# Kernel optimization log

Measured on AMD Instinct MI355X. Metric: run time of the kernel, lower is better.

## Reference

```python
import jax, jax.numpy as jnp
import numpy as np

HS = 2048   # hidden_size
NH = 16     # num_attention_heads
HD = HS // NH  # head_dim = 128
FD = 256    # feature_dim
EPS = 1e-5  # layer_norm_epsilon


def setup_inputs() -> dict:
    key = jax.random.key(0)
    ks = jax.random.split(key, 12)
    s = 0.02
    return {
        "hidden_states": jax.random.normal(ks[0], (2, 4096, HS), jnp.float32),
        "attention_mask": jnp.zeros((2, 4096), jnp.float32),
        "Wq": jax.random.normal(ks[1], (HS, HS), jnp.float32) * s,
        "bq": jnp.zeros((HS,), jnp.float32),
        "Wk": jax.random.normal(ks[2], (HS, HS), jnp.float32) * s,
        "bk": jnp.zeros((HS,), jnp.float32),
        "Wv": jax.random.normal(ks[3], (HS, HS), jnp.float32) * s,
        "bv": jnp.zeros((HS,), jnp.float32),
        "Wo": jax.random.normal(ks[4], (HS, HS), jnp.float32) * s,
        "bo": jnp.zeros((HS,), jnp.float32),
        "Wf1": jax.random.normal(ks[5], (HD, FD), jnp.float32) * s,
        "bf1": jnp.zeros((FD,), jnp.float32),
        "Wf2": jax.random.normal(ks[6], (FD, FD), jnp.float32) * s,
        "bf2": jnp.zeros((FD,), jnp.float32),
        "ln_g": jnp.ones((FD,), jnp.float32),
        "ln_b": jnp.zeros((FD,), jnp.float32),
    }


def reference(hidden_states, attention_mask, Wq, bq, Wk, bk, Wv, bv, Wo, bo,
              Wf1, bf1, Wf2, bf2, ln_g, ln_b):
    B, L, H = hidden_states.shape

    # QKV projections -> [B, NH, L, HD]
    q = (hidden_states @ Wq + bq).reshape(B, L, NH, HD).transpose(0, 2, 1, 3)
    k = (hidden_states @ Wk + bk).reshape(B, L, NH, HD).transpose(0, 2, 1, 3)
    v = (hidden_states @ Wv + bv).reshape(B, L, NH, HD).transpose(0, 2, 1, 3)

    # seq_len (4096) > linear_threshold (1024) -> linear attention branch
    def feature_map(x):  # Linear -> ReLU -> Linear -> LayerNorm
        h = jax.nn.relu(x @ Wf1 + bf1)
        h = h @ Wf2 + bf2
        mu = jnp.mean(h, axis=-1, keepdims=True)
        var = jnp.var(h, axis=-1, keepdims=True)  # biased, like torch LayerNorm
        return (h - mu) * jax.lax.rsqrt(var + EPS) * ln_g + ln_b

    q_feat = feature_map(q)  # [B, NH, L, FD]
    k_feat = feature_map(k)
    # attention_mask [B, L] -> k_feat * (1 + mask)
    k_feat = k_feat * (1.0 + attention_mask[:, None, :, None])

    kv = jnp.einsum('bhlf,bhld->bhfd', k_feat, v)          # [B, NH, FD, HD]
    attn = jnp.einsum('bhlf,bhfd->bhld', q_feat, kv)       # [B, NH, L, HD]
    k_sum = jnp.sum(k_feat, axis=2)                         # [B, NH, FD]
    denom = jnp.einsum('bhlf,bhf->bhl', q_feat, k_sum)[..., None]
    attn = attn / (denom + 1e-8)

    attn = attn.transpose(0, 2, 1, 3).reshape(B, L, H)
    return attn @ Wo + bo
```

## Files before the change

### kernel.cpp

```cpp
#include <hip/hip_runtime.h>

typedef unsigned short u16;
typedef unsigned int u32;
typedef __attribute__((ext_vector_type(8))) short bf16x8;
typedef __attribute__((ext_vector_type(4))) float f32x4;

#define B_ 2
#define L_ 4096
#define HS_ 2048
#define NH_ 16
#define HD_ 128
#define FD_ 256

__device__ __forceinline__ float bf2f(u16 u) { return __uint_as_float(((u32)u) << 16); }
__device__ __forceinline__ u16 f2bf(float f) {
    u32 x = __float_as_uint(f);
    return (u16)((x + 0x7fffu + ((x >> 16) & 1u)) >> 16);
}

__device__ __forceinline__ void llds16(const u16* g, u16* l) {
    __builtin_amdgcn_global_load_lds((const __attribute__((address_space(1))) void*)g,
                                     (__attribute__((address_space(3))) void*)l, 16, 0, 0);
}

__device__ __forceinline__ void gemm_mainloop(const u16* __restrict__ Ab, int lda,
                                              const u16* __restrict__ Bb, int ldb,
                                              int K, u16* As, u16* Bs, f32x4 (&acc)[4][4]) {
    const int tid  = threadIdx.x;
    const int lane = tid & 63;
    const int wave = tid >> 6;
    const int wm = wave >> 1, wn = wave & 1;

    f32x4 zero = {0.f, 0.f, 0.f, 0.f};
#pragma unroll
    for (int i = 0; i < 4; i++)
#pragma unroll
        for (int j = 0; j < 4; j++) acc[i][j] = zero;

    const int srow = lane >> 2;
    const int scol = (lane & 3) * 8;
    const u16* pa = Ab + (size_t)(wave * 32 + srow) * lda + scol;
    const u16* pb = Bb + (size_t)(wave * 32 + srow) * ldb + scol;
    u16* la = As + wave * 1024;
    u16* lb = Bs + wave * 1024;

    const int arow = (wm * 64 + (lane & 15)) * 32 + (lane >> 4) * 8;
    const int brow = (wn * 64 + (lane & 15)) * 32 + (lane >> 4) * 8;

    for (int k0 = 0; k0 < K; k0 += 32) {
        llds16(pa, la);
        llds16(pa + 16 * lda, la + 512);
        llds16(pb, lb);
        llds16(pb + 16 * ldb, lb + 512);
        pa += 32; pb += 32;
        __syncthreads();
        bf16x8 af[4], bg[4];
#pragma unroll
        for (int mt = 0; mt < 4; mt++) af[mt] = *(const bf16x8*)(As + arow + mt * 512);
#pragma unroll
        for (int nt = 0; nt < 4; nt++) bg[nt] = *(const bf16x8*)(Bs + brow + nt * 512);
#pragma unroll
        for (int mt = 0; mt < 4; mt++)
#pragma unroll
            for (int nt = 0; nt < 4; nt++)
                acc[mt][nt] = __builtin_amdgcn_mfma_f32_16x16x32_bf16(af[mt], bg[nt], acc[mt][nt], 0, 0, 0);
        __syncthreads();
    }
}

__global__ __launch_bounds__(256) void k_cvt(const float* __restrict__ src, u16* __restrict__ dst) {
    size_t i = ((size_t)blockIdx.x * 256 + threadIdx.x) * 8;
    float4 a = *(const float4*)(src + i);
    float4 b = *(const float4*)(src + i + 4);
    union { u16 h[8]; uint4 v; } o;
    o.h[0] = f2bf(a.x); o.h[1] = f2bf(a.y); o.h[2] = f2bf(a.z); o.h[3] = f2bf(a.w);
    o.h[4] = f2bf(b.x); o.h[5] = f2bf(b.y); o.h[6] = f2bf(b.z); o.h[7] = f2bf(b.w);
    *(uint4*)(dst + i) = o.v;
}

__global__ __launch_bounds__(256) void k_transpose(const float* Wq, const float* Wk, const float* Wv,
                                                   const float* Wo, const float* Wf1, const float* Wf2,
                                                   u16* Wqkv_t, u16* Wo_t, u16* Wf1_t, u16* Wf2_t) {
    const float* src; u16* dst; int R, C;
    switch (blockIdx.z) {
        case 0: src = Wq;  dst = Wqkv_t;                R = 2048; C = 2048; break;
        case 1: src = Wk;  dst = Wqkv_t + 2048 * 2048;  R = 2048; C = 2048; break;
        case 2: src = Wv;  dst = Wqkv_t + 2 * 2048 * 2048; R = 2048; C = 2048; break;
        case 3: src = Wo;  dst = Wo_t;                  R = 2048; C = 2048; break;
        case 4: src = Wf1; dst = Wf1_t;                 R = 128;  C = 256;  break;
        default: src = Wf2; dst = Wf2_t;                R = 256;  C = 256;  break;
    }
    int c0 = blockIdx.x * 32, r0 = blockIdx.y * 32;
    if (c0 >= C || r0 >= R) return;
    __shared__ u16 tile[32][33];
    int tx = threadIdx.x, ty = threadIdx.y;
    for (int i = ty; i < 32; i += 8) tile[i][tx] = f2bf(src[(size_t)(r0 + i) * C + c0 + tx]);
    __syncthreads();
    for (int i = ty; i < 32; i += 8) dst[(size_t)(c0 + i) * R + r0 + tx] = tile[tx][i];
}

__global__ __launch_bounds__(256) void k_gemm_qkv(const u16* __restrict__ X, const u16* __restrict__ Wt,
                                                  const float* __restrict__ bq, const float* __restrict__ bk,
                                                  const float* __restrict__ bv,
                                                  u16* __restrict__ qb, u16* __restrict__ kb, u16* __restrict__ vT) {
    __shared__ u16 As[4096], Bs[4096];
    f32x4 acc[4][4];
    const int mb = blockIdx.x * 128, nb = blockIdx.y * 128;
    gemm_mainloop(X + (size_t)mb * HS_, HS_, Wt + (size_t)nb * HS_, HS_, HS_, As, Bs, acc);
    const int lane = threadIdx.x & 63, wave = threadIdx.x >> 6;
    const int wm = wave >> 1, wn = wave & 1;
    const int n0 = nb + wn * 64 + (lane & 15);
    const int m0 = mb + wm * 64 + ((lane >> 4) << 2);
#pragma unroll
    for (int nt = 0; nt < 4; nt++) {
        int n = n0 + nt * 16;
        int which = n >> 11, col = n & 2047;
        const float* bias = (which == 0) ? bq : (which == 1 ? bk : bv);
        float bvv = bias[col];
        int h = col >> 7, d = col & 127;
        if (which == 2) {
#pragma unroll
            for (int mt = 0; mt < 4; mt++) {
                int m = m0 + mt * 16;
                int b = m >> 12, l = m & 4095;
                union { u16 h4[4]; uint2 v2; } pk;
#pragma unroll
                for (int r = 0; r < 4; r++) pk.h4[r] = f2bf(acc[mt][nt][r] + bvv);
                *(uint2*)(vT + ((size_t)((b * NH_ + h) * HD_ + d)) * L_ + l) = pk.v2;
            }
        } else {
            u16* dst = (which == 0) ? qb : kb;
#pragma unroll
            for (int mt = 0; mt < 4; mt++) {
#pragma unroll
                for (int r = 0; r < 4; r++) {
                    int m = m0 + mt * 16 + r;
                    int b = m >> 12, l = m & 4095;
                    dst[((size_t)((b * NH_ + h) * L_ + l)) * HD_ + d] = f2bf(acc[mt][nt][r] + bvv);
                }
            }
        }
    }
}

template <int MASKED, int TRANS>
__global__ __launch_bounds__(256) void k_feat(const u16* __restrict__ X,
                                              const u16* __restrict__ W1t, const float* __restrict__ b1,
                                              const u16* __restrict__ W2t, const float* __restrict__ b2,
                                              const float* __restrict__ g, const float* __restrict__ be,
                                              const float* __restrict__ mask,
                                              u16* __restrict__ feat) {
    __shared__ u16 As[64 * 32];
    __shared__ u16 Bs[256 * 32];
    __shared__ u16 H[64 * 264];
    __shared__ float MU[64], RS[64], FAC[64];
    const int tid = threadIdx.x, lane = tid & 63, wave = tid >> 6;
    const int mb = blockIdx.x * 64;

    const int srow = lane >> 2, scol = (lane & 3) * 8;
    const int arow_rd = (lane & 15);
    const int kgrp = (lane >> 4) * 8;

    f32x4 acc[4][4];
    f32x4 zero = {0.f, 0.f, 0.f, 0.f};
#pragma unroll
    for (int i = 0; i < 4; i++)
#pragma unroll
        for (int j = 0; j < 4; j++) acc[i][j] = zero;

    for (int k0 = 0; k0 < 128; k0 += 32) {
        llds16(X + (size_t)(mb + wave * 16 + srow) * 128 + k0 + scol, As + wave * 512);
#pragma unroll
        for (int i = 0; i < 4; i++)
            llds16(W1t + (size_t)((wave * 4 + i) * 16 + srow) * 128 + k0 + scol,
                   Bs + (wave * 4 + i) * 512);
        __syncthreads();
        bf16x8 af[4], bg[4];
#pragma unroll
        for (int mt = 0; mt < 4; mt++) af[mt] = *(const bf16x8*)(As + (mt * 16 + arow_rd) * 32 + kgrp);
#pragma unroll
        for (int nt = 0; nt < 4; nt++) bg[nt] = *(const bf16x8*)(Bs + (wave * 64 + nt * 16 + arow_rd) * 32 + kgrp);
#pragma unroll
        for (int mt = 0; mt < 4; mt++)
#pragma unroll
            for (int nt = 0; nt < 4; nt++)
                acc[mt][nt] = __builtin_amdgcn_mfma_f32_16x16x32_bf16(af[mt], bg[nt], acc[mt][nt], 0, 0, 0);
        __syncthreads();
    }
    {
        const int rbase = (lane >> 4) << 2;
#pragma unroll
        for (int nt = 0; nt < 4; nt++) {
            int n = wave * 64 + nt * 16 + (lane & 15);
            float bvv = b1[n];
#pragma unroll
            for (int mt = 0; mt < 4; mt++)
#pragma unroll
                for (int r = 0; r < 4; r++) {
                    float v = fmaxf(acc[mt][nt][r] + bvv, 0.f);
                    H[(mt * 16 + rbase + r) * 264 + n] = f2bf(v);
                }
            acc[0][nt] = zero; acc[1][nt] = zero; acc[2][nt] = zero; acc[3][nt] = zero;
        }
    }
    __syncthreads();

    for (int k0 = 0; k0 < 256; k0 += 32) {
#pragma unroll
        for (int i = 0; i < 4; i++)
            llds16(W2t + (size_t)((wave * 4 + i) * 16 + srow) * 256 + k0 + scol,
                   Bs + (wave * 4 + i) * 512);
        __syncthreads();
        bf16x8 af[4], bg[4];
#pragma unroll
        for (int mt = 0; mt < 4; mt++) af[mt] = *(const bf16x8*)(H + (mt * 16 + arow_rd) * 264 + k0 + kgrp);
#pragma unroll
        for (int nt = 0; nt < 4; nt++) bg[nt] = *(const bf16x8*)(Bs + (wave * 64 + nt * 16 + arow_rd) * 32 + kgrp);
#pragma unroll
        for (int mt = 0; mt < 4; mt++)
#pragma unroll
            for (int nt = 0; nt < 4; nt++)
                acc[mt][nt] = __builtin_amdgcn_mfma_f32_16x16x32_bf16(af[mt], bg[nt], acc[mt][nt], 0, 0, 0);
        __syncthreads();
    }
    {
        const int rbase = (lane >> 4) << 2;
#pragma unroll
        for (int nt = 0; nt < 4; nt++) {
            int n = wave * 64 + nt * 16 + (lane & 15);
            float bvv = b2[n];
#pragma unroll
            for (int mt = 0; mt < 4; mt++)
#pragma unroll
                for (int r = 0; r < 4; r++)
                    H[(mt * 16 + rbase + r) * 264 + n] = f2bf(acc[mt][nt][r] + bvv);
        }
    }
    __syncthreads();

    {
        for (int r = 0; r < 16; r++) {
            int row = wave * 16 + r;
            int j = lane * 4;
            uint2 u = *(const uint2*)(H + row * 264 + j);
            float x0 = bf2f((u16)(u.x & 0xffff)), x1 = bf2f((u16)(u.x >> 16));
            float x2 = bf2f((u16)(u.y & 0xffff)), x3 = bf2f((u16)(u.y >> 16));
            float s = x0 + x1 + x2 + x3;
            float ss = x0 * x0 + x1 * x1 + x2 * x2 + x3 * x3;
#pragma unroll
            for (int o = 32; o >= 1; o >>= 1) { s += __shfl_xor(s, o); ss += __shfl_xor(ss, o); }
            if (lane == 0) {
                float mu = s * (1.f / FD_);
                float var = ss * (1.f / FD_) - mu * mu;
                MU[row] = mu;
                RS[row] = rsqrtf(var + 1e-5f);
                float fac = 1.f;
                if (MASKED) {
                    int grow = mb + row;
                    int b = grow >> 16;
                    int l = grow & 4095;
                    fac = 1.f + mask[b * L_ + l];
                }
                FAC[row] = fac;
            }
        }
    }
    __syncthreads();

    if (!TRANS) {
        int j = lane * 4;
        float4 gg = *(const float4*)(g + j);
        float4 bb = *(const float4*)(be + j);
        for (int r = 0; r < 16; r++) {
            int row = wave * 16 + r;
            float mu = MU[row], rstd = RS[row], fac = FAC[row];
            uint2 u = *(const uint2*)(H + row * 264 + j);
            float x0 = bf2f((u16)(u.x & 0xffff)), x1 = bf2f((u16)(u.x >> 16));
            float x2 = bf2f((u16)(u.y & 0xffff)), x3 = bf2f((u16)(u.y >> 16));
            uint2 o2;
            o2.x = (u32)f2bf(((x0 - mu) * rstd * gg.x + bb.x) * fac) |
                   ((u32)f2bf(((x1 - mu) * rstd * gg.y + bb.y) * fac) << 16);
            o2.y = (u32)f2bf(((x2 - mu) * rstd * gg.z + bb.z) * fac) |
                   ((u32)f2bf(((x3 - mu) * rstd * gg.w + bb.w) * fac) << 16);
            *(uint2*)(feat + (size_t)(mb + row) * FD_ + j) = o2;
        }
    } else {
        int f = tid;
        int bh = mb >> 12, lb = mb & 4095;
        float gf = g[f], bf = be[f];
        u16* orow = feat + ((size_t)bh * FD_ + f) * L_ + lb;
        for (int lg = 0; lg < 64; lg += 8) {
            union { u16 h8[8]; uint4 v4; } pk;
#pragma unroll
            for (int j = 0; j < 8; j++) {
                int row = lg + j;
                float x = bf2f(H[row * 264 + f]);
                pk.h8[j] = f2bf(((x - MU[row]) * RS[row] * gf + bf) * FAC[row]);
            }
            *(uint4*)(orow + lg) = pk.v4;
        }
    }
}

__global__ __launch_bounds__(256) void k_ksum(const u16* __restrict__ kfT, float* __restrict__ ksum) {
    const int row = blockIdx.x;
    const int t = threadIdx.x, lane = t & 63, wave = t >> 6;
    const u16* p = kfT + (size_t)row * L_ + t * 16;
    uint4 a = *(const uint4*)p;
    uint4 b = *(const uint4*)(p + 8);
    float s = 0.f;
    const u32* w32 = (const u32*)&a;
#pragma unroll
    for (int i = 0; i < 4; i++) { s += bf2f((u16)(w32[i] & 0xffff)) + bf2f((u16)(w32[i] >> 16)); }
    const u32* w32b = (const u32*)&b;
#pragma unroll
    for (int i = 0; i < 4; i++) { s += bf2f((u16)(w32b[i] & 0xffff)) + bf2f((u16)(w32b[i] >> 16)); }
#pragma unroll
    for (int o = 32; o >= 1; o >>= 1) s += __shfl_xor(s, o);
    __shared__ float red[4];
    if (lane == 0) red[wave] = s;
    __syncthreads();
    if (t == 0) ksum[row] = red[0] + red[1] + red[2] + red[3];
}

__global__ __launch_bounds__(256) void k_gemm_kv(const u16* __restrict__ kfT, const u16* __restrict__ vT,
                                                 float* __restrict__ kvp) {
    __shared__ u16 As[4096], Bs[4096];
    f32x4 acc[4][4];
    const int mb = blockIdx.x * 128;
    const int ks = blockIdx.y;
    const int bh = blockIdx.z;
    gemm_mainloop(kfT + ((size_t)bh * FD_ + mb) * L_ + ks * 1024, L_,
                  vT + (size_t)bh * HD_ * L_ + ks * 1024, L_, 1024, As, Bs, acc);
    const int lane = threadIdx.x & 63, wave = threadIdx.x >> 6;
    const int wm = wave >> 1, wn = wave & 1;
    const int n0 = wn * 64 + (lane & 15);
    const int m0 = mb + wm * 64 + ((lane >> 4) << 2);
    float* o = kvp + (size_t)(ks * 32 + bh) * (FD_ * HD_);
#pragma unroll
    for (int nt = 0; nt < 4; nt++)
#pragma unroll
        for (int mt = 0; mt < 4; mt++)
#pragma unroll
            for (int r = 0; r < 4; r++)
                o[(size_t)(m0 + mt * 16 + r) * HD_ + n0 + nt * 16] = acc[mt][nt][r];
}

__global__ __launch_bounds__(256) void k_kvred(const float* __restrict__ kvp, u16* __restrict__ kvT) {
    const int p = blockIdx.x, bh = blockIdx.y, t = threadIdx.x;
    const int e0 = p * 4096 + t * 16;
    float s[16];
#pragma unroll
    for (int i = 0; i < 16; i++) s[i] = 0.f;
    for (int c = 0; c < 4; c++) {
        const float* src = kvp + ((size_t)(c * 32 + bh)) * 32768 + e0;
#pragma unroll
        for (int i = 0; i < 16; i += 4) {
            float4 vv = *(const float4*)(src + i);
            s[i] += vv.x; s[i + 1] += vv.y; s[i + 2] += vv.z; s[i + 3] += vv.w;
        }
    }
#pragma unroll
    for (int i = 0; i < 16; i++) {
        int e = e0 + i, fq = e >> 7, d = e & 127;
        kvT[((size_t)bh * HD_ + d) * FD_ + fq] = f2bf(s[i]);
    }
}

__global__ __launch_bounds__(256) void k_denom(const u16* __restrict__ qf, const float* __restrict__ ksum,
                                               float* __restrict__ denom) {
    const int lane = threadIdx.x & 63, wave = threadIdx.x >> 6;
    const size_t row = (size_t)blockIdx.x * 4 + wave;
    const int bh = (int)(row >> 12);
    uint2 u = *(const uint2*)(qf + row * FD_ + lane * 4);
    float4 kk = *(const float4*)(ksum + (size_t)bh * FD_ + lane * 4);
    float d = bf2f((u16)(u.x & 0xffff)) * kk.x + bf2f((u16)(u.x >> 16)) * kk.y
            + bf2f((u16)(u.y & 0xffff)) * kk.z + bf2f((u16)(u.y >> 16)) * kk.w;
#pragma unroll
    for (int o = 32; o >= 1; o >>= 1) d += __shfl_xor(d, o);
    if (lane == 0) denom[row] = d;
}

__global__ __launch_bounds__(256) void k_gemm_attn(const u16* __restrict__ qf, const u16* __restrict__ kvT,
                                                   const float* __restrict__ denom, u16* __restrict__ attn) {
    __shared__ u16 As[4096], Bs[4096];
    f32x4 acc[4][4];
    const int mb = blockIdx.x * 128;
    const int bh = blockIdx.y;
    gemm_mainloop(qf + ((size_t)bh * L_ + mb) * FD_, FD_, kvT + (size_t)bh * HD_ * FD_, FD_, FD_, As, Bs, acc);
    const int lane = threadIdx.x & 63, wave = threadIdx.x >> 6;
    const int wm = wave >> 1, wn = wave & 1;
    const int b = bh >> 4, h = bh & 15;
    const int n0 = wn * 64 + (lane & 15);
    const int m0 = mb + wm * 64 + ((lane >> 4) << 2);
#pragma unroll
    for (int mt = 0; mt < 4; mt++) {
#pragma unroll
        for (int r = 0; r < 4; r++) {
            int l = m0 + mt * 16 + r;
            float rden = 1.f / (denom[(size_t)bh * L_ + l] + 1e-8f);
            u16* orow = attn + ((size_t)(b * L_ + l) * HS_) + h * HD_;
#pragma unroll
            for (int nt = 0; nt < 4; nt++) orow[n0 + nt * 16] = f2bf(acc[mt][nt][r] * rden);
        }
    }
}

__global__ __launch_bounds__(256) void k_gemm_out(const u16* __restrict__ A, const u16* __restrict__ Wt,
                                                  const float* __restrict__ bo, float* __restrict__ out) {
    __shared__ u16 As[4096], Bs[4096];
    f32x4 acc[4][4];
    const int mb = blockIdx.x * 128, nb = blockIdx.y * 128;
    gemm_mainloop(A + (size_t)mb * HS_, HS_, Wt + (size_t)nb * HS_, HS_, HS_, As, Bs, acc);
    const int lane = threadIdx.x & 63, wave = threadIdx.x >> 6;
    const int wm = wave >> 1, wn = wave & 1;
    const int n0 = nb + wn * 64 + (lane & 15);
    const int m0 = mb + wm * 64 + ((lane >> 4) << 2);
#pragma unroll
    for (int nt = 0; nt < 4; nt++) {
        int n = n0 + nt * 16;
        float bvv = bo[n];
#pragma unroll
        for (int mt = 0; mt < 4; mt++)
#pragma unroll
            for (int r = 0; r < 4; r++)
                out[(size_t)(m0 + mt * 16 + r) * HS_ + n] = acc[mt][nt][r] + bvv;
    }
}

extern "C" void kernel_launch(void* const* d_in, const int* in_sizes, int n_in,
                              void* d_out, int out_size, void* d_ws, size_t ws_size,
                              hipStream_t stream) {
    const float* hs  = (const float*)d_in[0];
    const float* msk = (const float*)d_in[1];
    const float* Wq  = (const float*)d_in[2];  const float* bq  = (const float*)d_in[3];
    const float* Wk  = (const float*)d_in[4];  const float* bk  = (const float*)d_in[5];
    const float* Wv  = (const float*)d_in[6];  const float* bv  = (const float*)d_in[7];
    const float* Wo  = (const float*)d_in[8];  const float* bo  = (const float*)d_in[9];
    const float* Wf1 = (const float*)d_in[10]; const float* bf1 = (const float*)d_in[11];
    const float* Wf2 = (const float*)d_in[12]; const float* bf2 = (const float*)d_in[13];
    const float* lng = (const float*)d_in[14]; const float* lnb = (const float*)d_in[15];
    float* out = (float*)d_out;
    char* w = (char*)d_ws;

    u16* qfeat  = (u16*)(w + 0);
    u16* Wqkv_t = (u16*)(w + 0);
    u16* Xbf    = (u16*)(w + 25165824u);
    u16* kfT    = (u16*)(w + 67108864u);
    u16* qbuf   = (u16*)(w + 134217728u);
    float* kvp  = (float*)(w + 134217728u);
    u16* kbuf   = (u16*)(w + 167772160u);
    u16* attn   = (u16*)(w + 167772160u);
    u16* vT     = (u16*)(w + 201326592u);
    u16* Wo_t   = (u16*)(w + 234881024u);
    u16* Wf1_t  = (u16*)(w + 243269632u);
    u16* Wf2_t  = (u16*)(w + 243335168u);
    u16* kvT    = (u16*)(w + 243728384u);
    float* ksum = (float*)(w + 245825536u);
    float* denom = (float*)(w + 245858304u);

    k_cvt<<<dim3(8192), 256, 0, stream>>>(hs, Xbf);
    k_transpose<<<dim3(64, 64, 6), dim3(32, 8), 0, stream>>>(Wq, Wk, Wv, Wo, Wf1, Wf2,
                                                             Wqkv_t, Wo_t, Wf1_t, Wf2_t);
    k_gemm_qkv<<<dim3(64, 48), 256, 0, stream>>>(Xbf, Wqkv_t, bq, bk, bv, qbuf, kbuf, vT);
    k_feat<0, 0><<<dim3(2048), 256, 0, stream>>>(qbuf, Wf1_t, bf1, Wf2_t, bf2, lng, lnb, msk, qfeat);
    k_feat<1, 1><<<dim3(2048), 256, 0, stream>>>(kbuf, Wf1_t, bf1, Wf2_t, bf2, lng, lnb, msk, kfT);
    k_ksum<<<dim3(8192), 256, 0, stream>>>(kfT, ksum);
    k_gemm_kv<<<dim3(2, 4, 32), 256, 0, stream>>>(kfT, vT, kvp);
    k_kvred<<<dim3(8, 32), 256, 0, stream>>>(kvp, kvT);
    k_denom<<<dim3(32768), 256, 0, stream>>>(qfeat, ksum, denom);
    k_gemm_attn<<<dim3(32, 32), 256, 0, stream>>>(qfeat, kvT, denom, attn);
    k_gemm_out<<<dim3(64, 16), 256, 0, stream>>>(attn, Wo_t, bo, out);
}
```

Before: 811.5 us.

## Stage GEMM epilogues through LDS, swizzle blocks, fuse ksum into feature kernel

The QKV and attention GEMM epilogues now go through a padded shared-memory tile, so global stores become coalesced 16-byte writes instead of scattered 2-byte writes. The QKV and output GEMMs remap block indices into groups of eight row blocks to improve L2 reuse. The per-feature key sum is now accumulated in the transposed feature kernel and reduced by a small kernel, replacing a full re-read of kfT. The kv GEMM split-K count is doubled to 8 for more parallelism, which means more partial sums to reduce.

```diff
diff --git a/kernel.cpp b/kernel.cpp
--- a/kernel.cpp
+++ b/kernel.cpp
@@ -103,43 +103,57 @@
                                                   const float* __restrict__ bq, const float* __restrict__ bk,
                                                   const float* __restrict__ bv,
                                                   u16* __restrict__ qb, u16* __restrict__ kb, u16* __restrict__ vT) {
-    __shared__ u16 As[4096], Bs[4096];
+    __shared__ u16 S[128 * 132];
     f32x4 acc[4][4];
-    const int mb = blockIdx.x * 128, nb = blockIdx.y * 128;
-    gemm_mainloop(X + (size_t)mb * HS_, HS_, Wt + (size_t)nb * HS_, HS_, HS_, As, Bs, acc);
-    const int lane = threadIdx.x & 63, wave = threadIdx.x >> 6;
+    const int bid = blockIdx.y * 64 + blockIdx.x;
+    const int mblk = (bid / 384) * 8 + (bid & 7);
+    const int nblk = (bid >> 3) % 48;
+    const int mb = mblk * 128, nb = nblk * 128;
+    gemm_mainloop(X + (size_t)mb * HS_, HS_, Wt + (size_t)nb * HS_, HS_, HS_, S, S + 4096, acc);
+    const int tid = threadIdx.x, lane = tid & 63, wave = tid >> 6;
     const int wm = wave >> 1, wn = wave & 1;
-    const int n0 = nb + wn * 64 + (lane & 15);
-    const int m0 = mb + wm * 64 + ((lane >> 4) << 2);
-#pragma unroll
-    for (int nt = 0; nt < 4; nt++) {
-        int n = n0 + nt * 16;
-        int which = n >> 11, col = n & 2047;
-        const float* bias = (which == 0) ? bq : (which == 1 ? bk : bv);
-        float bvv = bias[col];
-        int h = col >> 7, d = col & 127;
-        if (which == 2) {
-#pragma unroll
-            for (int mt = 0; mt < 4; mt++) {
-                int m = m0 + mt * 16;
-                int b = m >> 12, l = m & 4095;
-                union { u16 h4[4]; uint2 v2; } pk;
-#pragma unroll
-                for (int r = 0; r < 4; r++) pk.h4[r] = f2bf(acc[mt][nt][r] + bvv);
-                *(uint2*)(vT + ((size_t)((b * NH_ + h) * HD_ + d)) * L_ + l) = pk.v2;
-            }
-        } else {
-            u16* dst = (which == 0) ? qb : kb;
-#pragma unroll
-            for (int mt = 0; mt < 4; mt++) {
-#pragma unroll
-                for (int r = 0; r < 4; r++) {
-                    int m = m0 + mt * 16 + r;
-                    int b = m >> 12, l = m & 4095;
-                    dst[((size_t)((b * NH_ + h) * L_ + l)) * HD_ + d] = f2bf(acc[mt][nt][r] + bvv);
-                }
-            }
-        }
+    const int which = nb >> 11;
+    const int col0 = nb & 2047;
+    const int h = col0 >> 7;
+    const int b = mb >> 12;
+    const int lb = mb & 4095;
+    const int bh = b * NH_ + h;
+    const float* bias = (which == 0) ? bq : (which == 1 ? bk : bv);
+    const int mloc = wm * 64 + ((lane >> 4) << 2);
+    const int nloc = wn * 64 + (lane & 15);
+    if (which < 2) {
+#pragma unroll
+        for (int nt = 0; nt < 4; nt++) {
+            float bvv = bias[col0 + nloc + nt * 16];
+#pragma unroll
+            for (int mt = 0; mt < 4; mt++)
+#pragma unroll
+                for (int r = 0; r < 4; r++)
+                    S[(mloc + mt * 16 + r) * 132 + nloc + nt * 16] = f2bf(acc[mt][nt][r] + bvv);
+        }
+    } else {
+#pragma unroll
+        for (int nt = 0; nt < 4; nt++) {
+            float bvv = bias[col0 + nloc + nt * 16];
+#pragma unroll
+            for (int mt = 0; mt < 4; mt++)
+#pragma unroll
+                for (int r = 0; r < 4; r++)
+                    S[(nloc + nt * 16) * 132 + mloc + mt * 16 + r] = f2bf(acc[mt][nt][r] + bvv);
+        }
+    }
+    __syncthreads();
+    u16* dst = (which == 0) ? qb : (which == 1 ? kb : vT);
+    const int c8 = (tid & 15) * 8;
+#pragma unroll
+    for (int it = 0; it < 8; it++) {
+        int row = (tid >> 4) + it * 16;
+        uint2 lo = *(const uint2*)(S + row * 132 + c8);
+        uint2 hi = *(const uint2*)(S + row * 132 + c8 + 4);
+        uint4 val = make_uint4(lo.x, lo.y, hi.x, hi.y);
+        u16* p = (which < 2) ? dst + ((size_t)bh * L_ + lb + row) * HD_ + c8
+                             : dst + ((size_t)bh * HD_ + row) * L_ + lb + c8;
+        *(uint4*)p = val;
     }
 }
 
@@ -149,7 +163,7 @@
                                               const u16* __restrict__ W2t, const float* __restrict__ b2,
                                               const float* __restrict__ g, const float* __restrict__ be,
                                               const float* __restrict__ mask,
-                                              u16* __restrict__ feat) {
+                                              u16* __restrict__ feat, float* __restrict__ ksp) {
     __shared__ u16 As[64 * 32];
     __shared__ u16 Bs[256 * 32];
     __shared__ u16 H[64 * 264];
@@ -289,38 +303,28 @@
         int bh = mb >> 12, lb = mb & 4095;
         float gf = g[f], bf = be[f];
         u16* orow = feat + ((size_t)bh * FD_ + f) * L_ + lb;
+        float fsum = 0.f;
         for (int lg = 0; lg < 64; lg += 8) {
             union { u16 h8[8]; uint4 v4; } pk;
 #pragma unroll
             for (int j = 0; j < 8; j++) {
                 int row = lg + j;
                 float x = bf2f(H[row * 264 + f]);
-                pk.h8[j] = f2bf(((x - MU[row]) * RS[row] * gf + bf) * FAC[row]);
+                float y = ((x - MU[row]) * RS[row] * gf + bf) * FAC[row];
+                fsum += y;
+                pk.h8[j] = f2bf(y);
             }
             *(uint4*)(orow + lg) = pk.v4;
         }
-    }
-}
-
-__global__ __launch_bounds__(256) void k_ksum(const u16* __restrict__ kfT, float* __restrict__ ksum) {
-    const int row = blockIdx.x;
-    const int t = threadIdx.x, lane = t & 63, wave = t >> 6;
-    const u16* p = kfT + (size_t)row * L_ + t * 16;
-    uint4 a = *(const uint4*)p;
-    uint4 b = *(const uint4*)(p + 8);
+        ksp[((size_t)bh * 64 + (lb >> 6)) * FD_ + f] = fsum;
+    }
+}
+
+__global__ __launch_bounds__(256) void k_ksum2(const float* __restrict__ ksp, float* __restrict__ ksum) {
+    const int bh = blockIdx.x, f = threadIdx.x;
     float s = 0.f;
-    const u32* w32 = (const u32*)&a;
-#pragma unroll
-    for (int i = 0; i < 4; i++) { s += bf2f((u16)(w32[i] & 0xffff)) + bf2f((u16)(w32[i] >> 16)); }
-    const u32* w32b = (const u32*)&b;
-#pragma unroll
-    for (int i = 0; i < 4; i++) { s += bf2f((u16)(w32b[i] & 0xffff)) + bf2f((u16)(w32b[i] >> 16)); }
-#pragma unroll
-    for (int o = 32; o >= 1; o >>= 1) s += __shfl_xor(s, o);
-    __shared__ float red[4];
-    if (lane == 0) red[wave] = s;
-    __syncthreads();
-    if (t == 0) ksum[row] = red[0] + red[1] + red[2] + red[3];
+    for (int i = 0; i < 64; i++) s += ksp[((size_t)bh * 64 + i) * FD_ + f];
+    ksum[(size_t)bh * FD_ + f] = s;
 }
 
 __global__ __launch_bounds__(256) void k_gemm_kv(const u16* __restrict__ kfT, const u16* __restrict__ vT,
@@ -330,8 +334,8 @@
     const int mb = blockIdx.x * 128;
     const int ks = blockIdx.y;
     const int bh = blockIdx.z;
-    gemm_mainloop(kfT + ((size_t)bh * FD_ + mb) * L_ + ks * 1024, L_,
-                  vT + (size_t)bh * HD_ * L_ + ks * 1024, L_, 1024, As, Bs, acc);
+    gemm_mainloop(kfT + ((size_t)bh * FD_ + mb) * L_ + ks * 512, L_,
+                  vT + (size_t)bh * HD_ * L_ + ks * 512, L_, 512, As, Bs, acc);
     const int lane = threadIdx.x & 63, wave = threadIdx.x >> 6;
     const int wm = wave >> 1, wn = wave & 1;
     const int n0 = wn * 64 + (lane & 15);
@@ -352,7 +356,7 @@
     float s[16];
 #pragma unroll
     for (int i = 0; i < 16; i++) s[i] = 0.f;
-    for (int c = 0; c < 4; c++) {
+    for (int c = 0; c < 8; c++) {
         const float* src = kvp + ((size_t)(c * 32 + bh)) * 32768 + e0;
 #pragma unroll
         for (int i = 0; i < 16; i += 4) {
@@ -383,26 +387,35 @@
 
 __global__ __launch_bounds__(256) void k_gemm_attn(const u16* __restrict__ qf, const u16* __restrict__ kvT,
                                                    const float* __restrict__ denom, u16* __restrict__ attn) {
-    __shared__ u16 As[4096], Bs[4096];
+    __shared__ u16 S[128 * 132];
     f32x4 acc[4][4];
     const int mb = blockIdx.x * 128;
     const int bh = blockIdx.y;
-    gemm_mainloop(qf + ((size_t)bh * L_ + mb) * FD_, FD_, kvT + (size_t)bh * HD_ * FD_, FD_, FD_, As, Bs, acc);
-    const int lane = threadIdx.x & 63, wave = threadIdx.x >> 6;
+    gemm_mainloop(qf + ((size_t)bh * L_ + mb) * FD_, FD_, kvT + (size_t)bh * HD_ * FD_, FD_, FD_, S, S + 4096, acc);
+    const int tid = threadIdx.x, lane = tid & 63, wave = tid >> 6;
     const int wm = wave >> 1, wn = wave & 1;
     const int b = bh >> 4, h = bh & 15;
-    const int n0 = wn * 64 + (lane & 15);
-    const int m0 = mb + wm * 64 + ((lane >> 4) << 2);
-#pragma unroll
-    for (int mt = 0; mt < 4; mt++) {
+    const int mloc = wm * 64 + ((lane >> 4) << 2);
+    const int nloc = wn * 64 + (lane & 15);
+#pragma unroll
+    for (int mt = 0; mt < 4; mt++)
 #pragma unroll
         for (int r = 0; r < 4; r++) {
-            int l = m0 + mt * 16 + r;
+            int l = mb + mloc + mt * 16 + r;
             float rden = 1.f / (denom[(size_t)bh * L_ + l] + 1e-8f);
-            u16* orow = attn + ((size_t)(b * L_ + l) * HS_) + h * HD_;
-#pragma unroll
-            for (int nt = 0; nt < 4; nt++) orow[n0 + nt * 16] = f2bf(acc[mt][nt][r] * rden);
-        }
+#pragma unroll
+            for (int nt = 0; nt < 4; nt++)
+                S[(mloc + mt * 16 + r) * 132 + nloc + nt * 16] = f2bf(acc[mt][nt][r] * rden);
+        }
+    __syncthreads();
+    const int c8 = (tid & 15) * 8;
+#pragma unroll
+    for (int it = 0; it < 8; it++) {
+        int row = (tid >> 4) + it * 16;
+        uint2 lo = *(const uint2*)(S + row * 132 + c8);
+        uint2 hi = *(const uint2*)(S + row * 132 + c8 + 4);
+        uint4 val = make_uint4(lo.x, lo.y, hi.x, hi.y);
+        *(uint4*)(attn + ((size_t)(b * L_ + mb + row)) * HS_ + h * HD_ + c8) = val;
     }
 }
 
@@ -410,7 +423,10 @@
                                                   const float* __restrict__ bo, float* __restrict__ out) {
     __shared__ u16 As[4096], Bs[4096];
     f32x4 acc[4][4];
-    const int mb = blockIdx.x * 128, nb = blockIdx.y * 128;
+    const int bid = blockIdx.y * 64 + blockIdx.x;
+    const int mblk = (bid / 128) * 8 + (bid & 7);
+    const int nblk = (bid >> 3) % 16;
+    const int mb = mblk * 128, nb = nblk * 128;
     gemm_mainloop(A + (size_t)mb * HS_, HS_, Wt + (size_t)nb * HS_, HS_, HS_, As, Bs, acc);
     const int lane = threadIdx.x & 63, wave = threadIdx.x >> 6;
     const int wm = wave >> 1, wn = wave & 1;
@@ -455,18 +471,19 @@
     u16* Wo_t   = (u16*)(w + 234881024u);
     u16* Wf1_t  = (u16*)(w + 243269632u);
     u16* Wf2_t  = (u16*)(w + 243335168u);
-    u16* kvT    = (u16*)(w + 243728384u);
-    float* ksum = (float*)(w + 245825536u);
-    float* denom = (float*)(w + 245858304u);
+    float* ksp  = (float*)(w + 243466240u);
+    u16* kvT    = (u16*)(w + 245563392u);
+    float* ksum = (float*)(w + 247660544u);
+    float* denom = (float*)(w + 247693312u);
 
     k_cvt<<<dim3(8192), 256, 0, stream>>>(hs, Xbf);
     k_transpose<<<dim3(64, 64, 6), dim3(32, 8), 0, stream>>>(Wq, Wk, Wv, Wo, Wf1, Wf2,
                                                              Wqkv_t, Wo_t, Wf1_t, Wf2_t);
     k_gemm_qkv<<<dim3(64, 48), 256, 0, stream>>>(Xbf, Wqkv_t, bq, bk, bv, qbuf, kbuf, vT);
-    k_feat<0, 0><<<dim3(2048), 256, 0, stream>>>(qbuf, Wf1_t, bf1, Wf2_t, bf2, lng, lnb, msk, qfeat);
-    k_feat<1, 1><<<dim3(2048), 256, 0, stream>>>(kbuf, Wf1_t, bf1, Wf2_t, bf2, lng, lnb, msk, kfT);
-    k_ksum<<<dim3(8192), 256, 0, stream>>>(kfT, ksum);
-    k_gemm_kv<<<dim3(2, 4, 32), 256, 0, stream>>>(kfT, vT, kvp);
+    k_feat<0, 0><<<dim3(2048), 256, 0, stream>>>(qbuf, Wf1_t, bf1, Wf2_t, bf2, lng, lnb, msk, qfeat, ksp);
+    k_feat<1, 1><<<dim3(2048), 256, 0, stream>>>(kbuf, Wf1_t, bf1, Wf2_t, bf2, lng, lnb, msk, kfT, ksp);
+    k_ksum2<<<dim3(32), 256, 0, stream>>>(ksp, ksum);
+    k_gemm_kv<<<dim3(2, 8, 32), 256, 0, stream>>>(kfT, vT, kvp);
     k_kvred<<<dim3(8, 32), 256, 0, stream>>>(kvp, kvT);
     k_denom<<<dim3(32768), 256, 0, stream>>>(qfeat, ksum, denom);
     k_gemm_attn<<<dim3(32, 32), 256, 0, stream>>>(qfeat, kvT, denom, attn);
```

Measured after the change: 807.1 us. Within noise of the previous version (-0.5%).
